# Kernel tuning notes

Hardware: AMD Instinct MI355X
Metric: run time of the kernel (lower is better)

Reference implementation:

```python
import jax, jax.numpy as jnp
import numpy as np

B, S, D, F, H = 64, 1024, 512, 256, 512


def setup_inputs() -> dict:
    key = jax.random.key(0)
    ks = jax.random.split(key, 13)
    sd = lambda fan_in: 1.0 / np.sqrt(fan_in)
    return {
        "x": jax.random.normal(ks[0], (B, D), jnp.float32),
        "encoder_outputs": jax.random.normal(ks[1], (B, S, D), jnp.float32),
        "field_embeddings": jax.random.normal(ks[2], (B, S, F), jnp.float32),
        # Dense params: field_embs_TIL (F->H), enc_outs_TIL (D->H),
        # state_fields_L (D->H), state_enc_outs_L (D->H), out_gate_L (2D->H)
        "W_f": jax.random.normal(ks[3], (F, H), jnp.float32) * sd(F),
        "b_f": jnp.zeros((H,), jnp.float32),
        "W_e": jax.random.normal(ks[4], (D, H), jnp.float32) * sd(D),
        "b_e": jnp.zeros((H,), jnp.float32),
        "W_sf": jax.random.normal(ks[5], (D, H), jnp.float32) * sd(D),
        "b_sf": jnp.zeros((H,), jnp.float32),
        "W_se": jax.random.normal(ks[6], (D, H), jnp.float32) * sd(D),
        "b_se": jnp.zeros((H,), jnp.float32),
        "W_g": jax.random.normal(ks[7], (2 * D, H), jnp.float32) * sd(2 * D),
        "b_g": jnp.zeros((H,), jnp.float32),
    }


def reference(x, encoder_outputs, field_embeddings,
              W_f, b_f, W_e, b_e, W_sf, b_sf, W_se, b_se, W_g, b_g):
    # calc_timestep_consts: seq-major layout [S, B, feat]
    enc_outs = jnp.transpose(encoder_outputs, (1, 0, 2))        # [S,B,D]
    fields = jnp.transpose(field_embeddings, (1, 0, 2))          # [S,B,F]
    fe_TI = jnp.tanh(fields @ W_f + b_f)                         # [S,B,H]
    eo_TI = jnp.tanh(enc_outs @ W_e + b_e)                       # [S,B,H]

    # call(x)
    state_tanh_f = jnp.tanh(x @ W_sf + b_sf)                     # [B,H]
    state_tanh_x = jnp.tanh(x @ W_se + b_se)                     # [B,H]

    score_enc_outs = jnp.einsum('bh,sbh->sb', state_tanh_x, eo_TI)  # [S,B]
    score_fields = jnp.einsum('bh,sbh->sb', state_tanh_f, fe_TI)    # [S,B]
    alphas = jax.nn.softmax(score_enc_outs, axis=0)
    betas = jax.nn.softmax(score_fields, axis=0)

    ab = alphas * betas
    gammas = ab / (1e-6 + jnp.sum(ab, axis=0, keepdims=True))    # [S,B]

    context = jnp.einsum('sb,sbd->bd', gammas, enc_outs)          # [B,D]
    out = jnp.tanh(jnp.concatenate([context, x], axis=-1) @ W_g + b_g)  # [B,H]
    return out, gammas
```

## Files before the change

### kernel.cpp

```cpp
#include <hip/hip_runtime.h>

#define B_ 64
#define S_ 1024
#define D_ 512
#define F_ 256
#define H_ 512

#define FLAGS_W  0
#define ST_F_W   16
#define ST_X_W   32784
#define SC_E_W   65552
#define SC_F_W   131088
#define WPEL_W   196624
#define WPFL_W   327696
#define GAM_W    327696
#define CTX_W    393232
#define WPEH_W   426000
#define WPFH_W   557072
#define CANARY_W 622608

typedef __attribute__((ext_vector_type(8))) short bf16x8;
typedef __attribute__((ext_vector_type(4))) short bf16x4;
typedef __attribute__((ext_vector_type(4))) float f32x4;
typedef unsigned short u16;
typedef unsigned int u32;

__device__ inline float bf2f(u16 u) {
  u32 i = ((u32)u) << 16;
  float f;
  __builtin_memcpy(&f, &i, 4);
  return f;
}
__device__ inline u16 f2bf(float f) {
  u32 i;
  __builtin_memcpy(&i, &f, 4);
  u32 r = i + 0x7fffu + ((i >> 16) & 1u);
  return (u16)(r >> 16);
}
__device__ inline void split_bf(float v, u16& h, u16& l) {
  u32 i;
  __builtin_memcpy(&i, &v, 4);
  h = (u16)(i >> 16);
  u32 hb = i & 0xFFFF0000u;
  float hf;
  __builtin_memcpy(&hf, &hb, 4);
  l = f2bf(v - hf);
}
__device__ inline float ldin(const void* p, size_t i, int f32) {
  return f32 ? ((const float*)p)[i] : bf2f(((const u16*)p)[i]);
}
__device__ inline void stout(void* p, size_t i, float v, int f32) {
  if (f32) ((float*)p)[i] = v;
  else ((u16*)p)[i] = f2bf(v);
}
__device__ inline float fast_tanh(float x) {
  float cx = fminf(15.f, fmaxf(-15.f, x));
  float e = __expf(2.f * cx);
  return (e - 1.f) * __builtin_amdgcn_rcpf(e + 1.f);
}

__global__ void probe_zero(const u16* __restrict__ We, u32* __restrict__ flags,
                           u32* __restrict__ canary, float* __restrict__ ctx) {
  if (blockIdx.x != 0) {
    int i = (blockIdx.x - 1) * 1024 + threadIdx.x * 4;
    *(f32x4*)&ctx[i] = (f32x4){0.f, 0.f, 0.f, 0.f};
    return;
  }
  __shared__ u32 cnt;
  if (threadIdx.x == 0) cnt = 0;
  __syncthreads();
  u32 local = 0;
  for (int i = threadIdx.x; i < 8192; i += 256) {
    u32 e = (We[i] >> 7) & 0xFF;
    if (e >= 134) ++local;
  }
  atomicAdd(&cnt, local);
  __syncthreads();
  if (threadIdx.x == 0) {
    flags[0] = (cnt > 128) ? 1u : 0u;
    for (int i = 1; i < 16; ++i) flags[i] = 0;
    canary[0] = 0xC0DE0001u; canary[1] = 0xC0DE0002u;
    canary[2] = 0xC0DE0003u; canary[3] = 0xC0DE0004u;
  }
}

__global__ void state_kernel(const void* __restrict__ x,
                             const void* __restrict__ Wsf, const void* __restrict__ bsf,
                             const void* __restrict__ Wse, const void* __restrict__ bse,
                             float* __restrict__ st_f, float* __restrict__ st_x,
                             const u32* __restrict__ flags) {
  const int f32 = flags[0];
  int tid = blockIdx.x * 256 + threadIdx.x;
  int h = tid & 511, b = (tid >> 9) & 63, which = tid >> 15;
  const void* W = which ? Wse : Wsf;
  const void* bias = which ? bse : bsf;
  float a[8] = {};
  for (int d = 0; d < D_; d += 8) {
#pragma unroll
    for (int j = 0; j < 8; ++j)
      a[j] += ldin(x, b * D_ + d + j, f32) * ldin(W, (size_t)(d + j) * H_ + h, f32);
  }
  float acc = ((a[0] + a[1]) + (a[2] + a[3])) + ((a[4] + a[5]) + (a[6] + a[7]));
  float v = fast_tanh(acc + ldin(bias, h, f32));
  (which ? st_x : st_f)[b * H_ + h] = v;
}

__global__ void pack2_kernel(const void* __restrict__ We, const void* __restrict__ Wf,
                             u16* __restrict__ WpEH, u16* __restrict__ WpEL,
                             u16* __restrict__ WpFH, u16* __restrict__ WpFL,
                             const u32* __restrict__ flags) {
  const int f32 = flags[0];
  int bid = blockIdx.x;
  const void* W;
  u16 *WpH, *WpL;
  int K, tb;
  if (bid < 128) { W = We; WpH = WpEH; WpL = WpEL; K = 512; tb = bid; }
  else           { W = Wf; WpH = WpFH; WpL = WpFL; K = 256; tb = bid - 128; }
  int t = tb * 256 + threadIdx.x;
  int lane = t & 63, tile = t >> 6;
  int kc = tile >> 5, nc = tile & 31;
  int kb = kc * 32 + ((lane >> 4) << 3);
  int nb = nc * 16 + (lane & 15);
  u16 vh[8], vl[8];
#pragma unroll
  for (int j = 0; j < 8; ++j) {
    float v = ldin(W, (size_t)(kb + j) * H_ + nb, f32);
    split_bf(v, vh[j], vl[j]);
  }
  size_t off = ((size_t)tile << 9) + (size_t)lane * 8;
#pragma unroll
  for (int j = 0; j < 8; ++j) {
    WpH[off + j] = vh[j];
    WpL[off + j] = vl[j];
  }
}

__global__ void __launch_bounds__(512, 2) score2_kernel(
    const void* __restrict__ enc, const void* __restrict__ fld,
    const u16* __restrict__ WpEH, const u16* __restrict__ WpEL,
    const u16* __restrict__ WpFH, const u16* __restrict__ WpFL,
    const void* __restrict__ be, const void* __restrict__ bfp,
    const float* __restrict__ stx, const float* __restrict__ stf,
    float* __restrict__ sce, float* __restrict__ scf,
    const u32* __restrict__ flags) {
  constexpr int KP = 128, LDK = KP + 8;
  __shared__ __attribute__((aligned(16))) short AsH[64 * LDK];
  __shared__ __attribute__((aligned(16))) short AsL[64 * LDK];
  __shared__ float scw[8][64];
  const int f32 = flags[0];
  const int tid = threadIdx.x;
  int bid = blockIdx.x;
  const int sel = bid >> 10;
  bid &= 1023;
  const void* A    = sel ? fld : enc;
  const u16* WpH   = sel ? WpFH : WpEH;
  const u16* WpL   = sel ? WpFL : WpEL;
  const void* bias = sel ? bfp : be;
  const float* st  = sel ? stf : stx;
  float* score     = sel ? scf : sce;
  const int K = sel ? F_ : D_;
  const int NPH = K >> 7, NK = NPH * 4;

  const int m0 = bid * 64;
  const int b = m0 >> 10, s0 = m0 & 1023;
  const int lane = tid & 63, wave = tid >> 6;
  const int ml = lane & 15, q = lane >> 4;
  const int nb = wave * 4;
  const bf16x8* wph = (const bf16x8*)WpH;
  const bf16x8* wpl = (const bf16x8*)WpL;
  const int sr = tid >> 5, scc = tid & 31;
  f32x4 pre[4];
  bf16x4 preb[4];

#define ISSUE_LOADS(PH)                                                              \
  do {                                                                               \
    if (f32) {                                                                       \
      _Pragma("unroll") for (int it = 0; it < 4; ++it)                               \
          pre[it] = *(const f32x4*)((const float*)A +                                \
                                    (size_t)(m0 + sr + 16 * it) * K + (PH)*KP + scc * 4); \
    } else {                                                                         \
      _Pragma("unroll") for (int it = 0; it < 4; ++it)                               \
          preb[it] = *(const bf16x4*)((const u16*)A +                                \
                                      (size_t)(m0 + sr + 16 * it) * K + (PH)*KP + scc * 4); \
    }                                                                                \
  } while (0)

#define WRITE_STAGE()                                                                \
  do {                                                                               \
    _Pragma("unroll") for (int it = 0; it < 4; ++it) {                               \
      float v[4];                                                                    \
      if (f32) {                                                                     \
        v[0] = pre[it][0]; v[1] = pre[it][1]; v[2] = pre[it][2]; v[3] = pre[it][3];  \
      } else {                                                                       \
        v[0] = bf2f((u16)preb[it][0]); v[1] = bf2f((u16)preb[it][1]);                \
        v[2] = bf2f((u16)preb[it][2]); v[3] = bf2f((u16)preb[it][3]);                \
      }                                                                              \
      bf16x4 hv, lv;                                                                 \
      _Pragma("unroll") for (int j = 0; j < 4; ++j) {                                \
        u16 hh, ll;                                                                  \
        split_bf(v[j], hh, ll);                                                      \
        hv[j] = (short)hh;                                                           \
        lv[j] = (short)ll;                                                           \
      }                                                                              \
      *(bf16x4*)&AsH[(sr + 16 * it) * LDK + scc * 4] = hv;                           \
      *(bf16x4*)&AsL[(sr + 16 * it) * LDK + scc * 4] = lv;                           \
    }                                                                                \
  } while (0)

#define LOAD_B(DH, DL, KCG)                                                          \
  do {                                                                               \
    _Pragma("unroll") for (int ns = 0; ns < 4; ++ns) {                               \
      size_t widx = (size_t)((KCG)*32 + nb + ns) * 64 + lane;                        \
      DH[ns] = wph[widx];                                                            \
      DL[ns] = wpl[widx];                                                            \
    }                                                                                \
  } while (0)

  f32x4 acc[4][4] = {};
  bf16x8 bh[4], bl[4], bhn[4], bln[4];
  ISSUE_LOADS(0);
  WRITE_STAGE();
  LOAD_B(bh, bl, 0);
  __syncthreads();
  for (int ph = 0; ph < NPH; ++ph) {
    if (ph + 1 < NPH) ISSUE_LOADS(ph + 1);
#pragma unroll
    for (int kc = 0; kc < KP / 32; ++kc) {
      const int kcg = ph * (KP / 32) + kc;
      const int kcn = (kcg + 1 < NK) ? (kcg + 1) : kcg;
      LOAD_B(bhn, bln, kcn);
      bf16x8 ah[4], al[4];
#pragma unroll
      for (int ms = 0; ms < 4; ++ms) {
        ah[ms] = *(const bf16x8*)&AsH[(ms * 16 + ml) * LDK + kc * 32 + q * 8];
        al[ms] = *(const bf16x8*)&AsL[(ms * 16 + ml) * LDK + kc * 32 + q * 8];
      }
      __builtin_amdgcn_s_setprio(1);
#pragma unroll
      for (int ms = 0; ms < 4; ++ms)
#pragma unroll
        for (int ns = 0; ns < 4; ++ns) {
          acc[ms][ns] = __builtin_amdgcn_mfma_f32_16x16x32_bf16(ah[ms], bh[ns], acc[ms][ns], 0, 0, 0);
          acc[ms][ns] = __builtin_amdgcn_mfma_f32_16x16x32_bf16(al[ms], bh[ns], acc[ms][ns], 0, 0, 0);
          acc[ms][ns] = __builtin_amdgcn_mfma_f32_16x16x32_bf16(ah[ms], bl[ns], acc[ms][ns], 0, 0, 0);
        }
      __builtin_amdgcn_s_setprio(0);
#pragma unroll
      for (int ns = 0; ns < 4; ++ns) { bh[ns] = bhn[ns]; bl[ns] = bln[ns]; }
    }
    if (ph + 1 < NPH) {
      __syncthreads();
      WRITE_STAGE();
      __syncthreads();
    }
  }
  float biasn[4], stn[4];
#pragma unroll
  for (int ns = 0; ns < 4; ++ns) {
    int n = (nb + ns) * 16 + ml;
    biasn[ns] = ldin(bias, n, f32);
    stn[ns] = st[b * H_ + n];
  }
#pragma unroll
  for (int ms = 0; ms < 4; ++ms) {
#pragma unroll
    for (int r = 0; r < 4; ++r) {
      float p = 0.f;
#pragma unroll
      for (int ns = 0; ns < 4; ++ns)
        p += fast_tanh(acc[ms][ns][r] + biasn[ns]) * stn[ns];
      p += __shfl_xor(p, 1);
      p += __shfl_xor(p, 2);
      p += __shfl_xor(p, 4);
      p += __shfl_xor(p, 8);
      if (ml == 0) scw[wave][ms * 16 + q * 4 + r] = p;
    }
  }
  __syncthreads();
  if (tid < 64) {
    float s = 0.f;
#pragma unroll
    for (int w = 0; w < 8; ++w) s += scw[w][tid];
    score[b * S_ + s0 + tid] = s;
  }
#undef ISSUE_LOADS
#undef WRITE_STAGE
#undef LOAD_B
}

__device__ inline float block_reduce_max(float v, float* red, int tid) {
#pragma unroll
  for (int off = 32; off >= 1; off >>= 1) v = fmaxf(v, __shfl_xor(v, off));
  if ((tid & 63) == 0) red[tid >> 6] = v;
  __syncthreads();
  v = fmaxf(fmaxf(red[0], red[1]), fmaxf(red[2], red[3]));
  __syncthreads();
  return v;
}
__device__ inline float block_reduce_sum(float v, float* red, int tid) {
#pragma unroll
  for (int off = 32; off >= 1; off >>= 1) v += __shfl_xor(v, off);
  if ((tid & 63) == 0) red[tid >> 6] = v;
  __syncthreads();
  v = red[0] + red[1] + red[2] + red[3];
  __syncthreads();
  return v;
}

__global__ void softmax_kernel(const float* __restrict__ se, const float* __restrict__ sf,
                               float* __restrict__ gam, void* __restrict__ dout,
                               u32* __restrict__ flags) {
  __shared__ float red[4];
  const int f32 = flags[0];
  int b = blockIdx.x, t = threadIdx.x;
  float e[4], f[4];
#pragma unroll
  for (int i = 0; i < 4; ++i) {
    e[i] = se[b * S_ + t + 256 * i];
    f[i] = sf[b * S_ + t + 256 * i];
    if (!(fabsf(e[i]) < 1e4f) || !(fabsf(f[i]) < 1e4f)) flags[4] = 1;
  }
  float me = block_reduce_max(fmaxf(fmaxf(e[0], e[1]), fmaxf(e[2], e[3])), red, t);
  float mf = block_reduce_max(fmaxf(fmaxf(f[0], f[1]), fmaxf(f[2], f[3])), red, t);
  float sume = 0.f, sumf = 0.f;
#pragma unroll
  for (int i = 0; i < 4; ++i) {
    e[i] = __expf(e[i] - me);
    sume += e[i];
    f[i] = __expf(f[i] - mf);
    sumf += f[i];
  }
  sume = block_reduce_sum(sume, red, t);
  sumf = block_reduce_sum(sumf, red, t);
  float g[4], tot = 0.f;
#pragma unroll
  for (int i = 0; i < 4; ++i) {
    g[i] = (e[i] / sume) * (f[i] / sumf);
    tot += g[i];
  }
  tot = block_reduce_sum(tot, red, t);
  float scale = 1.f / (1e-6f + tot);
#pragma unroll
  for (int i = 0; i < 4; ++i) {
    int s = t + 256 * i;
    float gv = g[i] * scale;
    gam[b * S_ + s] = gv;
    stout(dout, (size_t)B_ * H_ + (size_t)s * B_ + b, gv, f32);
  }
}

__global__ void ctx_kernel(const float* __restrict__ gam, const void* __restrict__ enc,
                           float* __restrict__ ctx, const u32* __restrict__ flags) {
  const int f32 = flags[0];
  int b = blockIdx.x >> 4, sc = blockIdx.x & 15;
  int t = threadIdx.x, d0 = t * 2;
  float a0 = 0.f, a1 = 0.f;
#pragma unroll 4
  for (int s = sc * 64; s < sc * 64 + 64; ++s) {
    float g = gam[b * S_ + s];
    size_t base = ((size_t)(b * S_ + s)) * D_ + d0;
    a0 += g * ldin(enc, base, f32);
    a1 += g * ldin(enc, base + 1, f32);
  }
  atomicAdd(&ctx[b * D_ + d0], a0);
  atomicAdd(&ctx[b * D_ + d0 + 1], a1);
}

__global__ void out_kernel(const float* __restrict__ ctx, const void* __restrict__ x,
                           const void* __restrict__ Wg, const void* __restrict__ bg,
                           void* __restrict__ dout, const u32* __restrict__ flags,
                           const u32* __restrict__ canary) {
  const int f32 = flags[0];
  int tid = blockIdx.x * 256 + threadIdx.x;
  int h = tid & 511, b = tid >> 9;
  float a0 = 0.f, a1 = 0.f, a2 = 0.f, a3 = 0.f;
  for (int d = 0; d < D_; d += 4) {
    a0 += ctx[b * D_ + d]     * ldin(Wg, (size_t)d * H_ + h, f32);
    a1 += ctx[b * D_ + d + 1] * ldin(Wg, (size_t)(d + 1) * H_ + h, f32);
    a2 += ctx[b * D_ + d + 2] * ldin(Wg, (size_t)(d + 2) * H_ + h, f32);
    a3 += ctx[b * D_ + d + 3] * ldin(Wg, (size_t)(d + 3) * H_ + h, f32);
  }
  for (int d = 0; d < D_; d += 4) {
    a0 += ldin(x, b * D_ + d, f32)     * ldin(Wg, (size_t)(D_ + d) * H_ + h, f32);
    a1 += ldin(x, b * D_ + d + 1, f32) * ldin(Wg, (size_t)(D_ + d + 1) * H_ + h, f32);
    a2 += ldin(x, b * D_ + d + 2, f32) * ldin(Wg, (size_t)(D_ + d + 2) * H_ + h, f32);
    a3 += ldin(x, b * D_ + d + 3, f32) * ldin(Wg, (size_t)(D_ + d + 3) * H_ + h, f32);
  }
  float acc = (a0 + a1) + (a2 + a3);
  float v = fast_tanh(acc + ldin(bg, h, f32));
  if (tid == 0) {
    u32 code = 0;
    if (canary[0] != 0xC0DE0001u || canary[1] != 0xC0DE0002u ||
        canary[2] != 0xC0DE0003u || canary[3] != 0xC0DE0004u) code += 32;
    if (flags[4]) code += 64;
    if (code) v = (float)code;
  }
  stout(dout, (size_t)b * H_ + h, v, f32);
}

extern "C" void kernel_launch(void* const* d_in, const int* in_sizes, int n_in,
                              void* d_out, int out_size, void* d_ws, size_t ws_size,
                              hipStream_t stream) {
  const void* x    = d_in[0];
  const void* enc  = d_in[1];
  const void* fld  = d_in[2];
  const void* W_f  = d_in[3];
  const void* b_f  = d_in[4];
  const void* W_e  = d_in[5];
  const void* b_e  = d_in[6];
  const void* W_sf = d_in[7];
  const void* b_sf = d_in[8];
  const void* W_se = d_in[9];
  const void* b_se = d_in[10];
  const void* W_g  = d_in[11];
  const void* b_g  = d_in[12];

  float* ws    = (float*)d_ws;
  u32* flags   = (u32*)(ws + FLAGS_W);
  float* st_f  = ws + ST_F_W;
  float* st_x  = ws + ST_X_W;
  float* sc_e  = ws + SC_E_W;
  float* sc_f  = ws + SC_F_W;
  float* gam   = ws + GAM_W;
  float* ctx   = ws + CTX_W;
  u16* WpEH    = (u16*)(ws + WPEH_W);
  u16* WpEL    = (u16*)(ws + WPEL_W);
  u16* WpFH    = (u16*)(ws + WPFH_W);
  u16* WpFL    = (u16*)(ws + WPFL_W);
  u32* canary  = (u32*)(ws + CANARY_W);

  probe_zero<<<33, 256, 0, stream>>>((const u16*)W_e, flags, canary, ctx);
  state_kernel<<<256, 256, 0, stream>>>(x, W_sf, b_sf, W_se, b_se, st_f, st_x, flags);
  pack2_kernel<<<192, 256, 0, stream>>>(W_e, W_f, WpEH, WpEL, WpFH, WpFL, flags);
  score2_kernel<<<2048, 512, 0, stream>>>(enc, fld, WpEH, WpEL, WpFH, WpFL,
                                          b_e, b_f, st_x, st_f, sc_e, sc_f, flags);
  softmax_kernel<<<64, 256, 0, stream>>>(sc_e, sc_f, gam, d_out, flags);
  ctx_kernel<<<1024, 256, 0, stream>>>(gam, enc, ctx, flags);
  out_kernel<<<128, 256, 0, stream>>>(ctx, x, W_g, b_g, d_out, flags, canary);
}
```

Baseline: 567.2 us.

## Fuse prep kernels, double-buffer score LDS staging, fuse softmax into context

Merges the dtype probe, state projection and weight packing into one prep kernel, with each block redoing a smaller dtype probe locally. Double-buffers the A tile in shared memory of the score GEMM so the next stage is written mid-loop, and speeds up the hi/lo bf16 split with perm and packed-convert instructions. Fuses softmax into the context kernel, so each of the 16 blocks per batch recomputes the softmax instead of round-tripping gammas through global memory. This cuts launches and barriers at the cost of redundant softmax work and double the LDS use.

```diff
diff --git a/kernel.cpp b/kernel.cpp
--- a/kernel.cpp
+++ b/kernel.cpp
@@ -13,7 +13,6 @@
 #define SC_F_W   131088
 #define WPEL_W   196624
 #define WPFL_W   327696
-#define GAM_W    327696
 #define CTX_W    393232
 #define WPEH_W   426000
 #define WPFH_W   557072
@@ -46,6 +45,11 @@
   __builtin_memcpy(&hf, &hb, 4);
   l = f2bf(v - hf);
 }
+__device__ inline u32 cvt_pk_bf16(float a, float b) {
+  u32 r;
+  asm("v_cvt_pk_bf16_f32 %0, %1, %2" : "=v"(r) : "v"(a), "v"(b));
+  return r;
+}
 __device__ inline float ldin(const void* p, size_t i, int f32) {
   return f32 ? ((const float*)p)[i] : bf2f(((const u16*)p)[i]);
 }
@@ -59,65 +63,64 @@
   return (e - 1.f) * __builtin_amdgcn_rcpf(e + 1.f);
 }
 
-__global__ void probe_zero(const u16* __restrict__ We, u32* __restrict__ flags,
-                           u32* __restrict__ canary, float* __restrict__ ctx) {
-  if (blockIdx.x != 0) {
-    int i = (blockIdx.x - 1) * 1024 + threadIdx.x * 4;
-    *(f32x4*)&ctx[i] = (f32x4){0.f, 0.f, 0.f, 0.f};
-    return;
-  }
+__global__ void prep_kernel(const u16* __restrict__ We16,
+                            const void* __restrict__ We, const void* __restrict__ Wf,
+                            const void* __restrict__ x,
+                            const void* __restrict__ Wsf, const void* __restrict__ bsf,
+                            const void* __restrict__ Wse, const void* __restrict__ bse,
+                            float* __restrict__ st_f, float* __restrict__ st_x,
+                            u16* __restrict__ WpEH, u16* __restrict__ WpEL,
+                            u16* __restrict__ WpFH, u16* __restrict__ WpFL,
+                            u32* __restrict__ flags, u32* __restrict__ canary,
+                            float* __restrict__ ctx) {
   __shared__ u32 cnt;
   if (threadIdx.x == 0) cnt = 0;
   __syncthreads();
   u32 local = 0;
-  for (int i = threadIdx.x; i < 8192; i += 256) {
-    u32 e = (We[i] >> 7) & 0xFF;
+  for (int i = threadIdx.x; i < 1024; i += 256) {
+    u32 e = (We16[i] >> 7) & 0xFF;
     if (e >= 134) ++local;
   }
-  atomicAdd(&cnt, local);
-  __syncthreads();
-  if (threadIdx.x == 0) {
-    flags[0] = (cnt > 128) ? 1u : 0u;
-    for (int i = 1; i < 16; ++i) flags[i] = 0;
-    canary[0] = 0xC0DE0001u; canary[1] = 0xC0DE0002u;
-    canary[2] = 0xC0DE0003u; canary[3] = 0xC0DE0004u;
-  }
-}
-
-__global__ void state_kernel(const void* __restrict__ x,
-                             const void* __restrict__ Wsf, const void* __restrict__ bsf,
-                             const void* __restrict__ Wse, const void* __restrict__ bse,
-                             float* __restrict__ st_f, float* __restrict__ st_x,
-                             const u32* __restrict__ flags) {
-  const int f32 = flags[0];
-  int tid = blockIdx.x * 256 + threadIdx.x;
-  int h = tid & 511, b = (tid >> 9) & 63, which = tid >> 15;
-  const void* W = which ? Wse : Wsf;
-  const void* bias = which ? bse : bsf;
-  float a[8] = {};
-  for (int d = 0; d < D_; d += 8) {
-#pragma unroll
-    for (int j = 0; j < 8; ++j)
-      a[j] += ldin(x, b * D_ + d + j, f32) * ldin(W, (size_t)(d + j) * H_ + h, f32);
-  }
-  float acc = ((a[0] + a[1]) + (a[2] + a[3])) + ((a[4] + a[5]) + (a[6] + a[7]));
-  float v = fast_tanh(acc + ldin(bias, h, f32));
-  (which ? st_x : st_f)[b * H_ + h] = v;
-}
-
-__global__ void pack2_kernel(const void* __restrict__ We, const void* __restrict__ Wf,
-                             u16* __restrict__ WpEH, u16* __restrict__ WpEL,
-                             u16* __restrict__ WpFH, u16* __restrict__ WpFL,
-                             const u32* __restrict__ flags) {
-  const int f32 = flags[0];
-  int bid = blockIdx.x;
+  if (local) atomicAdd(&cnt, local);
+  __syncthreads();
+  const int f32 = cnt > 64;
+  const int bid = blockIdx.x, t = threadIdx.x;
+
+  if (bid < 32) {
+    int i = bid * 1024 + t * 4;
+    *(f32x4*)&ctx[i] = (f32x4){0.f, 0.f, 0.f, 0.f};
+    if (bid == 0 && t == 0) {
+      flags[0] = (u32)f32;
+      for (int i2 = 1; i2 < 16; ++i2) flags[i2] = 0;
+      canary[0] = 0xC0DE0001u; canary[1] = 0xC0DE0002u;
+      canary[2] = 0xC0DE0003u; canary[3] = 0xC0DE0004u;
+    }
+    return;
+  }
+  if (bid < 288) {
+    int tid = (bid - 32) * 256 + t;
+    int h = tid & 511, b = (tid >> 9) & 63, which = tid >> 15;
+    const void* W = which ? Wse : Wsf;
+    const void* bias = which ? bse : bsf;
+    float a[8] = {};
+    for (int d = 0; d < D_; d += 8) {
+#pragma unroll
+      for (int j = 0; j < 8; ++j)
+        a[j] += ldin(x, b * D_ + d + j, f32) * ldin(W, (size_t)(d + j) * H_ + h, f32);
+    }
+    float acc = ((a[0] + a[1]) + (a[2] + a[3])) + ((a[4] + a[5]) + (a[6] + a[7]));
+    float v = fast_tanh(acc + ldin(bias, h, f32));
+    (which ? st_x : st_f)[b * H_ + h] = v;
+    return;
+  }
+  int tb = bid - 288;
   const void* W;
   u16 *WpH, *WpL;
-  int K, tb;
-  if (bid < 128) { W = We; WpH = WpEH; WpL = WpEL; K = 512; tb = bid; }
-  else           { W = Wf; WpH = WpFH; WpL = WpFL; K = 256; tb = bid - 128; }
-  int t = tb * 256 + threadIdx.x;
-  int lane = t & 63, tile = t >> 6;
+  int K;
+  if (tb < 128) { W = We; WpH = WpEH; WpL = WpEL; K = 512; }
+  else          { W = Wf; WpH = WpFH; WpL = WpFL; K = 256; tb -= 128; }
+  int tg = tb * 256 + t;
+  int lane = tg & 63, tile = tg >> 6;
   int kc = tile >> 5, nc = tile & 31;
   int kb = kc * 32 + ((lane >> 4) << 3);
   int nb = nc * 16 + (lane & 15);
@@ -144,8 +147,8 @@
     float* __restrict__ sce, float* __restrict__ scf,
     const u32* __restrict__ flags) {
   constexpr int KP = 128, LDK = KP + 8;
-  __shared__ __attribute__((aligned(16))) short AsH[64 * LDK];
-  __shared__ __attribute__((aligned(16))) short AsL[64 * LDK];
+  __shared__ __attribute__((aligned(16))) short AsH[2][64 * LDK];
+  __shared__ __attribute__((aligned(16))) short AsL[2][64 * LDK];
   __shared__ float scw[8][64];
   const int f32 = flags[0];
   const int tid = threadIdx.x;
@@ -185,25 +188,35 @@
     }                                                                                \
   } while (0)
 
-#define WRITE_STAGE()                                                                \
+#define WRITE_STAGE(BUF)                                                             \
   do {                                                                               \
     _Pragma("unroll") for (int it = 0; it < 4; ++it) {                               \
-      float v[4];                                                                    \
+      u32 iv[4];                                                                     \
+      float vf[4];                                                                   \
       if (f32) {                                                                     \
-        v[0] = pre[it][0]; v[1] = pre[it][1]; v[2] = pre[it][2]; v[3] = pre[it][3];  \
+        _Pragma("unroll") for (int j = 0; j < 4; ++j) {                              \
+          vf[j] = pre[it][j];                                                        \
+          __builtin_memcpy(&iv[j], &vf[j], 4);                                       \
+        }                                                                            \
       } else {                                                                       \
-        v[0] = bf2f((u16)preb[it][0]); v[1] = bf2f((u16)preb[it][1]);                \
-        v[2] = bf2f((u16)preb[it][2]); v[3] = bf2f((u16)preb[it][3]);                \
+        _Pragma("unroll") for (int j = 0; j < 4; ++j) {                              \
+          iv[j] = ((u32)(u16)preb[it][j]) << 16;                                     \
+          __builtin_memcpy(&vf[j], &iv[j], 4);                                       \
+        }                                                                            \
       }                                                                              \
-      bf16x4 hv, lv;                                                                 \
+      u32 h01 = __builtin_amdgcn_perm(iv[1], iv[0], 0x07060302u);                    \
+      u32 h23 = __builtin_amdgcn_perm(iv[3], iv[2], 0x07060302u);                    \
+      float hf[4];                                                                   \
       _Pragma("unroll") for (int j = 0; j < 4; ++j) {                                \
-        u16 hh, ll;                                                                  \
-        split_bf(v[j], hh, ll);                                                      \
-        hv[j] = (short)hh;                                                           \
-        lv[j] = (short)ll;                                                           \
+        u32 hb = iv[j] & 0xFFFF0000u;                                                \
+        __builtin_memcpy(&hf[j], &hb, 4);                                            \
       }                                                                              \
-      *(bf16x4*)&AsH[(sr + 16 * it) * LDK + scc * 4] = hv;                           \
-      *(bf16x4*)&AsL[(sr + 16 * it) * LDK + scc * 4] = lv;                           \
+      u32 l01 = cvt_pk_bf16(vf[0] - hf[0], vf[1] - hf[1]);                           \
+      u32 l23 = cvt_pk_bf16(vf[2] - hf[2], vf[3] - hf[3]);                           \
+      u32* dH = (u32*)&AsH[BUF][(sr + 16 * it) * LDK + scc * 4];                     \
+      u32* dL = (u32*)&AsL[BUF][(sr + 16 * it) * LDK + scc * 4];                     \
+      dH[0] = h01; dH[1] = h23;                                                      \
+      dL[0] = l01; dL[1] = l23;                                                      \
     }                                                                                \
   } while (0)
 
@@ -219,22 +232,25 @@
   f32x4 acc[4][4] = {};
   bf16x8 bh[4], bl[4], bhn[4], bln[4];
   ISSUE_LOADS(0);
-  WRITE_STAGE();
+  WRITE_STAGE(0);
+  ISSUE_LOADS(1);
   LOAD_B(bh, bl, 0);
   __syncthreads();
   for (int ph = 0; ph < NPH; ++ph) {
-    if (ph + 1 < NPH) ISSUE_LOADS(ph + 1);
-#pragma unroll
-    for (int kc = 0; kc < KP / 32; ++kc) {
-      const int kcg = ph * (KP / 32) + kc;
+    const int cur = ph & 1, nxt = cur ^ 1;
+#pragma unroll
+    for (int kc = 0; kc < 4; ++kc) {
+      const int kcg = ph * 4 + kc;
       const int kcn = (kcg + 1 < NK) ? (kcg + 1) : kcg;
       LOAD_B(bhn, bln, kcn);
       bf16x8 ah[4], al[4];
 #pragma unroll
       for (int ms = 0; ms < 4; ++ms) {
-        ah[ms] = *(const bf16x8*)&AsH[(ms * 16 + ml) * LDK + kc * 32 + q * 8];
-        al[ms] = *(const bf16x8*)&AsL[(ms * 16 + ml) * LDK + kc * 32 + q * 8];
+        ah[ms] = *(const bf16x8*)&AsH[cur][(ms * 16 + ml) * LDK + kc * 32 + q * 8];
+        al[ms] = *(const bf16x8*)&AsL[cur][(ms * 16 + ml) * LDK + kc * 32 + q * 8];
       }
+      if (kc == 2 && ph + 1 < NPH) WRITE_STAGE(nxt);
+      if (kc == 3 && ph + 2 < NPH) ISSUE_LOADS(ph + 2);
       __builtin_amdgcn_s_setprio(1);
 #pragma unroll
       for (int ms = 0; ms < 4; ++ms)
@@ -248,11 +264,7 @@
 #pragma unroll
       for (int ns = 0; ns < 4; ++ns) { bh[ns] = bhn[ns]; bl[ns] = bln[ns]; }
     }
-    if (ph + 1 < NPH) {
-      __syncthreads();
-      WRITE_STAGE();
-      __syncthreads();
-    }
+    __syncthreads();
   }
   float biasn[4], stn[4];
 #pragma unroll
@@ -307,19 +319,23 @@
   return v;
 }
 
-__global__ void softmax_kernel(const float* __restrict__ se, const float* __restrict__ sf,
-                               float* __restrict__ gam, void* __restrict__ dout,
-                               u32* __restrict__ flags) {
+__global__ void ctx2_kernel(const float* __restrict__ se, const float* __restrict__ sf,
+                            const void* __restrict__ enc, float* __restrict__ ctx,
+                            void* __restrict__ dout, u32* __restrict__ flags) {
   __shared__ float red[4];
+  __shared__ float gl[S_];
   const int f32 = flags[0];
-  int b = blockIdx.x, t = threadIdx.x;
+  int b = blockIdx.x >> 4, sc = blockIdx.x & 15;
+  int t = threadIdx.x;
   float e[4], f[4];
+  int bad = 0;
 #pragma unroll
   for (int i = 0; i < 4; ++i) {
     e[i] = se[b * S_ + t + 256 * i];
     f[i] = sf[b * S_ + t + 256 * i];
-    if (!(fabsf(e[i]) < 1e4f) || !(fabsf(f[i]) < 1e4f)) flags[4] = 1;
-  }
+    if (!(fabsf(e[i]) < 1e4f) || !(fabsf(f[i]) < 1e4f)) bad = 1;
+  }
+  if (bad && sc == 0) flags[4] = 1;
   float me = block_reduce_max(fmaxf(fmaxf(e[0], e[1]), fmaxf(e[2], e[3])), red, t);
   float mf = block_reduce_max(fmaxf(fmaxf(f[0], f[1]), fmaxf(f[2], f[3])), red, t);
   float sume = 0.f, sumf = 0.f;
@@ -344,23 +360,18 @@
   for (int i = 0; i < 4; ++i) {
     int s = t + 256 * i;
     float gv = g[i] * scale;
-    gam[b * S_ + s] = gv;
-    stout(dout, (size_t)B_ * H_ + (size_t)s * B_ + b, gv, f32);
-  }
-}
-
-__global__ void ctx_kernel(const float* __restrict__ gam, const void* __restrict__ enc,
-                           float* __restrict__ ctx, const u32* __restrict__ flags) {
-  const int f32 = flags[0];
-  int b = blockIdx.x >> 4, sc = blockIdx.x & 15;
-  int t = threadIdx.x, d0 = t * 2;
+    gl[s] = gv;
+    if (sc == 0) stout(dout, (size_t)B_ * H_ + (size_t)s * B_ + b, gv, f32);
+  }
+  __syncthreads();
+  int d0 = t * 2;
   float a0 = 0.f, a1 = 0.f;
 #pragma unroll 4
   for (int s = sc * 64; s < sc * 64 + 64; ++s) {
-    float g = gam[b * S_ + s];
+    float gv = gl[s];
     size_t base = ((size_t)(b * S_ + s)) * D_ + d0;
-    a0 += g * ldin(enc, base, f32);
-    a1 += g * ldin(enc, base + 1, f32);
+    a0 += gv * ldin(enc, base, f32);
+    a1 += gv * ldin(enc, base + 1, f32);
   }
   atomicAdd(&ctx[b * D_ + d0], a0);
   atomicAdd(&ctx[b * D_ + d0 + 1], a1);
@@ -421,7 +432,6 @@
   float* st_x  = ws + ST_X_W;
   float* sc_e  = ws + SC_E_W;
   float* sc_f  = ws + SC_F_W;
-  float* gam   = ws + GAM_W;
   float* ctx   = ws + CTX_W;
   u16* WpEH    = (u16*)(ws + WPEH_W);
   u16* WpEL    = (u16*)(ws + WPEL_W);
@@ -429,12 +439,11 @@
   u16* WpFL    = (u16*)(ws + WPFL_W);
   u32* canary  = (u32*)(ws + CANARY_W);
 
-  probe_zero<<<33, 256, 0, stream>>>((const u16*)W_e, flags, canary, ctx);
-  state_kernel<<<256, 256, 0, stream>>>(x, W_sf, b_sf, W_se, b_se, st_f, st_x, flags);
-  pack2_kernel<<<192, 256, 0, stream>>>(W_e, W_f, WpEH, WpEL, WpFH, WpFL, flags);
+  prep_kernel<<<480, 256, 0, stream>>>((const u16*)W_e, W_e, W_f, x,
+                                       W_sf, b_sf, W_se, b_se, st_f, st_x,
+                                       WpEH, WpEL, WpFH, WpFL, flags, canary, ctx);
   score2_kernel<<<2048, 512, 0, stream>>>(enc, fld, WpEH, WpEL, WpFH, WpFL,
                                           b_e, b_f, st_x, st_f, sc_e, sc_f, flags);
-  softmax_kernel<<<64, 256, 0, stream>>>(sc_e, sc_f, gam, d_out, flags);
-  ctx_kernel<<<1024, 256, 0, stream>>>(gam, enc, ctx, flags);
+  ctx2_kernel<<<1024, 256, 0, stream>>>(sc_e, sc_f, enc, ctx, d_out, flags);
   out_kernel<<<128, 256, 0, stream>>>(ctx, x, W_g, b_g, d_out, flags, canary);
 }
```

Result: no change. 560.7 us (-1.1%).
